# Kernel optimization log

Measured on AMD Instinct MI355X. Metric: run time of the kernel, lower is better.

## Reference

```python
import jax, jax.numpy as jnp
import numpy as np
import math

H = 16
LORA_SCALING = 16 / 8  # alpha / r
NEG_INF = -1e30

def _alibi_slopes(n_heads):
    start = 2.0 ** (-(2.0 ** (-(math.log2(n_heads) - 3))))
    return jnp.asarray([start * start ** i for i in range(n_heads)], dtype=jnp.float32)

def setup_inputs() -> dict:
    key = jax.random.key(0)
    ks = jax.random.split(key, 11)
    B, T, E, r = 4, 2048, 1024, 8
    d = {
        'x':  jax.random.normal(ks[0], (B, T, E), jnp.float32),
        'Wq': jax.random.normal(ks[1], (E, E), jnp.float32) * (E ** -0.5),
        'Aq': jax.random.normal(ks[2], (E, r), jnp.float32) * 0.01,
        'Bq': jax.random.normal(ks[3], (r, E), jnp.float32) * 0.01,
        'Wk': jax.random.normal(ks[4], (E, E), jnp.float32) * (E ** -0.5),
        'Ak': jax.random.normal(ks[5], (E, r), jnp.float32) * 0.01,
        'Bk': jax.random.normal(ks[6], (r, E), jnp.float32) * 0.01,
        'Wv': jax.random.normal(ks[7], (E, E), jnp.float32) * (E ** -0.5),
        'Av': jax.random.normal(ks[8], (E, r), jnp.float32) * 0.01,
        'Bv': jax.random.normal(ks[9], (r, E), jnp.float32) * 0.01,
        'Wp': jax.random.normal(ks[10], (E, E), jnp.float32) * (E ** -0.5),
    }
    return d

def _lora(x, W, A, Bm):
    # nn.Linear: x @ W.T ; LoRA: x @ B.T @ A.T * scaling
    return x @ W.T + ((x @ Bm.T) @ A.T) * LORA_SCALING

def reference(x, Wq, Aq, Bq, Wk, Ak, Bk, Wv, Av, Bv, Wp):
    B, T, E = x.shape
    dh = E // H
    q = _lora(x, Wq, Aq, Bq).reshape(B, T, H, dh).transpose(0, 2, 1, 3)  # [B,H,T,dh]
    k = _lora(x, Wk, Ak, Bk).reshape(B, T, H, dh).transpose(0, 2, 1, 3)
    v = _lora(x, Wv, Av, Bv).reshape(B, T, H, dh).transpose(0, 2, 1, 3)
    s = jnp.einsum('bhqd,bhkd->bhqk', q, k) / jnp.sqrt(jnp.float32(dh))
    i = jnp.arange(T)[:, None]
    j = jnp.arange(T)[None, :]
    slopes = _alibi_slopes(H)
    bias = slopes[:, None, None] * (i - j).astype(jnp.float32)  # [H,T,T]
    s = s + bias[None]
    s = jnp.where(j[None, None] <= i[None, None], s, NEG_INF)  # causal mask
    out = jnp.einsum('bhqk,bhkd->bhqd', jax.nn.softmax(s, axis=-1), v)
    out = out.transpose(0, 2, 1, 3).reshape(B, T, E)
    return out @ Wp.T  # dropout is identity in eval
```

## Files before the change

kernel.cpp:

```cpp
#include <hip/hip_runtime.h>

typedef unsigned short u16;
typedef unsigned int u32;
typedef u16  u16x8 __attribute__((ext_vector_type(8)));
typedef u16  u16x4 __attribute__((ext_vector_type(4)));
typedef u32  u32x4 __attribute__((ext_vector_type(4)));
typedef __bf16 bf16x2 __attribute__((ext_vector_type(2)));
typedef __bf16 bf16x8 __attribute__((ext_vector_type(8)));
typedef float f32x4 __attribute__((ext_vector_type(4)));
typedef float f32x16 __attribute__((ext_vector_type(16)));

__constant__ int KBW[16]  = {0,1,1,2,3,5,7,10,14,20,28,40,56,80,113,160};

__constant__ unsigned char RANKTBL[256] = {
  0xBF,0xCF,0xDF,0xEF,0xFF,
  0xBE,0xCE,0xDE,0xEE,0xFE,
  0xAE,0xAF,
  0xAD,0xBD,0xCD,0xDD,0xED,0xFD,
  0xAC,0xBC,0xCC,0xDC,0xEC,0xFC,
  0xAB,0xBB,0xCB,0xDB,0xEB,0xFB,
  0xAA,0xBA,0xCA,0xDA,0xEA,0xFA,
  0x9A,0x9B,0x9C,0x9D,0x9E,0x9F,
  0x99,0xA9,0xB9,0xC9,0xD9,0xE9,0xF9,
  0x98,0xA8,0xB8,0xC8,0xD8,0xE8,0xF8,
  0x97,0xA7,0xB7,0xC7,0xD7,0xE7,0xF7,
  0x87,0x88,0x89,0x8A,0x8B,0x8C,0x8D,0x8E,0x8F,
  0x86,0x96,0xA6,0xB6,0xC6,0xD6,0xE6,0xF6,
  0x85,0x95,0xA5,0xB5,0xC5,0xD5,0xE5,0xF5,
  0x75,0x76,0x77,0x78,0x79,0x7A,0x7B,0x7C,0x7D,0x7E,0x7F,
  0x74,0x84,0x94,0xA4,0xB4,0xC4,0xD4,0xE4,0xF4,
  0x63,0x64,0x65,0x66,0x67,0x68,0x69,0x6A,0x6B,0x6C,0x6D,0x6E,0x6F,
  0x73,0x83,0x93,0xA3,0xB3,0xC3,0xD3,0xE3,0xF3,
  0x52,0x53,0x54,0x55,0x56,0x57,0x58,0x59,0x5A,0x5B,0x5C,0x5D,0x5E,0x5F,
  0x62,0x72,0x82,0x92,0xA2,0xB2,0xC2,0xD2,0xE2,0xF2,
  0x41,0x42,0x43,0x44,0x45,0x46,0x47,0x48,0x49,0x4A,0x4B,0x4C,0x4D,0x4E,0x4F,
  0x51,0x61,0x71,0x81,0x91,0xA1,0xB1,0xC1,0xD1,0xE1,0xF1,
  0x31,0x32,0x33,0x34,0x35,0x36,0x37,0x38,0x39,0x3A,0x3B,0x3C,0x3D,0x3E,0x3F,
  0x10,0x11,0x12,0x13,0x14,0x15,0x16,0x17,0x18,0x19,0x1A,0x1B,0x1C,0x1D,0x1E,0x1F,
  0x20,0x21,0x22,0x23,0x24,0x25,0x26,0x27,0x28,0x29,0x2A,0x2B,0x2C,0x2D,0x2E,0x2F,
  0x30,0x40,0x50,0x60,0x70,0x80,0x90,0xA0,0xB0,0xC0,0xD0,0xE0,0xF0,
  0x00,0x01,0x02,0x03,0x04,0x05,0x06,0x07,0x08,0x09,0x0A,0x0B,0x0C,0x0D,0x0E,0x0F
};

static __device__ __forceinline__ u16 f2bf(float f) {
  unsigned int u = __float_as_uint(f);
  u += 0x7FFFu + ((u >> 16) & 1u);
  return (u16)(u >> 16);
}

static __device__ __forceinline__ u32 packbf(float a, float b) {
  bf16x2 t;
  t[0] = (__bf16)a;
  t[1] = (__bf16)b;
  return __builtin_bit_cast(u32, t);
}

static __device__ __forceinline__ f32x4 mfma16(bf16x8 a, bf16x8 b, f32x4 c) {
  return __builtin_amdgcn_mfma_f32_16x16x32_bf16(a, b, c, 0, 0, 0);
}
static __device__ __forceinline__ f32x16 mfma32(bf16x8 a, bf16x8 b, f32x16 c) {
  return __builtin_amdgcn_mfma_f32_32x32x16_bf16(a, b, c, 0, 0, 0);
}

static __device__ __forceinline__ void gload16(const void* g, void* lds) {
  __builtin_amdgcn_global_load_lds(
      (const __attribute__((address_space(1))) unsigned int*)g,
      (__attribute__((address_space(3))) unsigned int*)lds, 16, 0, 0);
}

__global__ __launch_bounds__(256) void k_cast_x(const float* __restrict__ in,
                                                u16* __restrict__ out) {
  size_t i = (size_t)blockIdx.x * 256 + threadIdx.x;
  const float4* p = reinterpret_cast<const float4*>(in) + i * 2;
  float4 a = p[0], b = p[1];
  u16x8 r;
  r[0] = f2bf(a.x); r[1] = f2bf(a.y); r[2] = f2bf(a.z); r[3] = f2bf(a.w);
  r[4] = f2bf(b.x); r[5] = f2bf(b.y); r[6] = f2bf(b.z); r[7] = f2bf(b.w);
  *reinterpret_cast<u16x8*>(out + i * 8) = r;
}

__global__ __launch_bounds__(256) void k_fold_w(
    const float* __restrict__ Wq, const float* __restrict__ Aq, const float* __restrict__ Bq,
    const float* __restrict__ Wk, const float* __restrict__ Ak, const float* __restrict__ Bk,
    const float* __restrict__ Wv, const float* __restrict__ Av, const float* __restrict__ Bv,
    const float* __restrict__ Wp, u16* __restrict__ wqkv, u16* __restrict__ wp) {
  int n = blockIdx.x;
  int widx = n >> 10, nr = n & 1023;
  const float *W, *A, *Bm; u16* dst;
  if (widx == 0)      { W = Wq; A = Aq; Bm = Bq; dst = wqkv; }
  else if (widx == 1) { W = Wk; A = Ak; Bm = Bk; dst = wqkv + (1 << 20); }
  else if (widx == 2) { W = Wv; A = Av; Bm = Bv; dst = wqkv + (2 << 20); }
  else                { W = Wp; A = nullptr; Bm = nullptr; dst = wp; }
  int e0 = threadIdx.x * 4;
  float4 w = *reinterpret_cast<const float4*>(W + (size_t)nr * 1024 + e0);
  if (widx < 3) {
    float acx = 0.f, acy = 0.f, acz = 0.f, acw = 0.f;
#pragma unroll
    for (int r = 0; r < 8; r++) {
      float ar = A[nr * 8 + r];
      float4 bm = *reinterpret_cast<const float4*>(Bm + (size_t)r * 1024 + e0);
      acx += ar * bm.x; acy += ar * bm.y; acz += ar * bm.z; acw += ar * bm.w;
    }
    w.x += 2.0f * acx; w.y += 2.0f * acy; w.z += 2.0f * acz; w.w += 2.0f * acw;
  }
  u16x4 r4; r4[0] = f2bf(w.x); r4[1] = f2bf(w.y); r4[2] = f2bf(w.z); r4[3] = f2bf(w.w);
  *reinterpret_cast<u16x4*>(dst + (size_t)nr * 1024 + e0) = r4;
}

template<int OUTF32>
__global__ __launch_bounds__(512) void k_gemm8(const u16* __restrict__ Ag,
                                               const u16* __restrict__ Bg,
                                               void* __restrict__ C,
                                               int K, int N, int lda, int gx) {
  __shared__ __align__(16) u16 As[2][8192];
  __shared__ __align__(16) u16 Bs[2][16384];
  const int tid = threadIdx.x;
  const int wid = tid >> 6, lane = tid & 63;
  const int l15 = lane & 15, lg = lane >> 4;
  const int wr = wid >> 2, wc = wid & 3;
  const int nwg = gridDim.x, cpx = nwg >> 3;
  const int bid = (int)blockIdx.x;
  const int sid = (bid & 7) * cpx + (bid >> 3);
  const int m0 = (sid % gx) * 128, n0 = (sid / gx) * 256;

  const int lrow = lane >> 3;
  const int lslot = lane & 7;

  f32x4 acc[4][4];
#pragma unroll
  for (int i = 0; i < 4; i++)
#pragma unroll
    for (int j = 0; j < 4; j++) acc[i][j] = (f32x4)0.0f;

  auto stageA = [&](int d, int t) {
#pragma unroll
    for (int i = 0; i < 2; i++) {
      int row = i * 64 + wid * 8 + lrow;
      int sc = (lslot ^ (row & 7)) << 3;
      gload16(Ag + (size_t)(m0 + row) * lda + t * 64 + sc,
              &As[d][(i * 64 + wid * 8) * 64]);
    }
  };
  auto stageB = [&](int d, int t) {
#pragma unroll
    for (int i = 0; i < 4; i++) {
      int row = i * 64 + wid * 8 + lrow;
      int sc = (lslot ^ (row & 7)) << 3;
      gload16(Bg + (size_t)(n0 + row) * K + t * 64 + sc,
              &Bs[d][(i * 64 + wid * 8) * 64]);
    }
  };
  auto ldsA = [&](int d, int m, int kk) {
    int rr = wr * 64 + m * 16 + l15;
    return *reinterpret_cast<const bf16x8*>(&As[d][rr * 64 + (((kk * 4 + lg) ^ (rr & 7)) << 3)]);
  };
  auto ldsB = [&](int d, int n, int kk) {
    int rr = wc * 64 + n * 16 + l15;
    return *reinterpret_cast<const bf16x8*>(&Bs[d][rr * 64 + (((kk * 4 + lg) ^ (rr & 7)) << 3)]);
  };

  bf16x8 fa[4][2], fb[4][2];
  auto quad = [&](int mh, int nh) {
    __builtin_amdgcn_s_setprio(1);
#pragma unroll
    for (int m = 0; m < 2; m++)
#pragma unroll
      for (int n = 0; n < 2; n++)
#pragma unroll
        for (int kk = 0; kk < 2; kk++)
          acc[mh * 2 + m][nh * 2 + n] =
              mfma16(fa[mh * 2 + m][kk], fb[nh * 2 + n][kk], acc[mh * 2 + m][nh * 2 + n]);
    __builtin_amdgcn_s_setprio(0);
  };

#define MIDBAR do { asm volatile("s_barrier" ::: "memory"); \
                    asm volatile("s_waitcnt lgkmcnt(0)" ::: "memory"); } while (0)
#define ENDBAR asm volatile("s_barrier" ::: "memory")

  stageB(0, 0); stageA(0, 0); stageB(1, 1); stageA(1, 1);
  asm volatile("s_waitcnt vmcnt(0)" ::: "memory");
  asm volatile("s_barrier" ::: "memory");

  const int niter = K >> 7;
  for (int it = 0; it < niter; ++it) {
    const bool st = (it + 1 < niter);
    const int T2 = 2 * it + 2;
#pragma unroll
    for (int d = 0; d < 2; ++d) {
#pragma unroll
      for (int m = 0; m < 2; m++)
#pragma unroll
        for (int kk = 0; kk < 2; kk++) fa[m][kk] = ldsA(d, m, kk);
#pragma unroll
      for (int n = 0; n < 2; n++)
#pragma unroll
        for (int kk = 0; kk < 2; kk++) fb[n][kk] = ldsB(d, n, kk);
      MIDBAR; quad(0, 0); ENDBAR;
#pragma unroll
      for (int n = 2; n < 4; n++)
#pragma unroll
        for (int kk = 0; kk < 2; kk++) fb[n][kk] = ldsB(d, n, kk);
      MIDBAR; quad(0, 1); ENDBAR;
#pragma unroll
      for (int m = 2; m < 4; m++)
#pragma unroll
        for (int kk = 0; kk < 2; kk++) fa[m][kk] = ldsA(d, m, kk);
      if (st) stageB(d, T2 + d);
      MIDBAR; quad(1, 1); ENDBAR;
      if (st) stageA(d, T2 + d);
      MIDBAR; quad(1, 0);
      if (st) asm volatile("s_waitcnt vmcnt(6)" ::: "memory");
      else    asm volatile("s_waitcnt vmcnt(0)" ::: "memory");
      ENDBAR;
    }
  }
#undef MIDBAR
#undef ENDBAR

  const int rbase = m0 + wr * 64, cbase = n0 + wc * 64;
#pragma unroll
  for (int m = 0; m < 4; m++)
#pragma unroll
    for (int n = 0; n < 4; n++)
#pragma unroll
      for (int j = 0; j < 4; j++) {
        int r  = rbase + m * 16 + lg * 4 + j;
        int cc = cbase + n * 16 + l15;
        if constexpr (OUTF32) {
          reinterpret_cast<float*>(C)[(size_t)r * N + cc] = acc[m][n][j];
        } else {
          reinterpret_cast<u16*>(C)[(size_t)r * N + cc] = f2bf(acc[m][n][j]);
        }
      }
}

__global__ __launch_bounds__(256) void k_vt(const u16* __restrict__ qkv,
                                            u16* __restrict__ vt) {
  __shared__ __align__(16) u16 tile[64 * 64];
  const int tb = blockIdx.x, h = blockIdx.y, b = blockIdx.z;
  const int tid = threadIdx.x;
  const size_t rb = (size_t)b * 2048;
  const int hv = 2048 + h * 64;
#pragma unroll
  for (int p = 0; p < 2; p++) {
    int r = p * 32 + (tid >> 3);
    int c = (tid & 7) * 8;
    u16x8 v = *reinterpret_cast<const u16x8*>(qkv + (rb + tb * 64 + r) * 3072 + hv + c);
    int slot = (c >> 3) ^ (r & 7) ^ ((r >> 3) & 7);
    *reinterpret_cast<u16x8*>(tile + r * 64 + slot * 8) = v;
  }
  __syncthreads();
#pragma unroll
  for (int p = 0; p < 2; p++) {
    int d = p * 32 + (tid >> 3);
    int t0 = (tid & 7) * 8;
    u16x8 v;
#pragma unroll
    for (int j = 0; j < 8; j++) {
      int r = t0 + j;
      int slot = (d >> 3) ^ (r & 7) ^ ((r >> 3) & 7);
      v[j] = tile[r * 64 + slot * 8 + (d & 7)];
    }
    *reinterpret_cast<u16x8*>(vt + ((size_t)(b * 16 + h) * 64 + d) * 2048 + tb * 64 + t0) = v;
  }
}

__global__ __launch_bounds__(256) void k_attn(const u16* __restrict__ qkv,
                                              const u16* __restrict__ vt,
                                              u16* __restrict__ aout) {
  __shared__ __align__(16) u16 Kl[2][64 * 64];
  __shared__ __align__(16) u16 Vl[2][64 * 64];
  const int tid = threadIdx.x, wave = tid >> 6, lane = tid & 63;
  const int l31 = lane & 31, half = lane >> 5;
  const int i = (int)blockIdx.x;
  const int b = i & 3, p = i >> 2;
  const int k4 = p >> 6, j4 = p & 63;
  const int ridx = (k4 == 0) ? j4 : (k4 == 1) ? 127 - j4 : (k4 == 2) ? 128 + j4 : 255 - j4;
  const int hqv = RANKTBL[ridx];
  const int h = hqv >> 4, qb = hqv & 15;
  const int rb = b * 2048;
  const int hq = h * 64, hk = 1024 + h * 64;
  const int bh64 = (b * 16 + h) * 64;
  const int qB = qb * 128;
  const int q0w = qB + wave * 32;
  const int q = q0w + l31;

  bf16x8 qf[4];
#pragma unroll
  for (int c = 0; c < 4; c++)
    qf[c] = *reinterpret_cast<const bf16x8*>(qkv + (size_t)(rb + q) * 3072 + hq + c * 16 + half * 8);

  const float slope2 = exp2f(-0.5f * (float)(h + 1)) * 1.44269504f;
  const float c0 = 0.18033688f;

  const int kend = min(2 * qb + 1, KBW[h]);

  float mrun = -1e30f, lrun = 0.f;
  f32x16 o0 = (f32x16)0.0f, o1 = (f32x16)0.0f;

  auto stage = [&](int kvr, int dst) {
#pragma unroll
    for (int i2 = 0; i2 < 2; i2++) {
      int row = (i2 * 4 + wave) * 8 + (lane >> 3);
      int scol = ((lane & 7) ^ (row & 7)) << 3;
      gload16(qkv + (size_t)(rb + kvr + row) * 3072 + hk + scol, &Kl[dst][(i2 * 4 + wave) * 512]);
      gload16(vt + (size_t)(bh64 + row) * 2048 + kvr + scol,     &Vl[dst][(i2 * 4 + wave) * 512]);
    }
  };

  stage(0, 0);
  __syncthreads();

  int bfi = 0;
  for (int kb = 0; kb <= kend; ++kb, bfi ^= 1) {
    const int kvr = kb * 64;
    if (kb < kend) stage(kvr + 64, bfi ^ 1);

    if (kvr <= q0w + 31) {
      f32x16 s[2];
#pragma unroll
      for (int t = 0; t < 2; t++) s[t] = (f32x16)0.0f;
      __builtin_amdgcn_s_setprio(1);
#pragma unroll
      for (int t = 0; t < 2; t++) {
        int r = t * 32 + l31;
#pragma unroll
        for (int cc = 0; cc < 4; cc++) {
          bf16x8 kf = *reinterpret_cast<const bf16x8*>(
              &Kl[bfi][r * 64 + (((cc * 2 + half) ^ (r & 7)) << 3)]);
          s[t] = mfma32(kf, qf[cc], s[t]);
        }
      }
      __builtin_amdgcn_s_setprio(0);

      const bool domask = (kvr + 63 > q0w);
      const int qrel = q - kvr - half * 4;
      const float qb0 = slope2 * (float)qrel;
      const float qb1 = qb0 - slope2 * 32.0f;
      float mt = -1e30f;
      if (domask) {
#pragma unroll
        for (int t = 0; t < 2; t++) {
          const float qbt = t ? qb1 : qb0;
          const int qmt = t ? (qrel - 32) : qrel;
#pragma unroll
          for (int r = 0; r < 16; r++) {
            const int krel = (r & 3) + 8 * (r >> 2);
            float val = fmaf(s[t][r], c0, fmaf(-slope2, (float)krel, qbt));
            val = (krel <= qmt) ? val : -3.0e38f;
            s[t][r] = val;
            mt = fmaxf(mt, val);
          }
        }
      } else {
#pragma unroll
        for (int t = 0; t < 2; t++) {
          const float qbt = t ? qb1 : qb0;
#pragma unroll
          for (int r = 0; r < 16; r += 2) {
            const int k0 = (r & 3) + 8 * (r >> 2);
            const int k1 = ((r + 1) & 3) + 8 * ((r + 1) >> 2);
            float v0 = fmaf(s[t][r],     c0, fmaf(-slope2, (float)k0, qbt));
            float v1 = fmaf(s[t][r + 1], c0, fmaf(-slope2, (float)k1, qbt));
            s[t][r] = v0; s[t][r + 1] = v1;
            mt = fmaxf(mt, fmaxf(v0, v1));
          }
        }
      }
      mt = fmaxf(mt, __shfl_xor(mt, 32));

      if (__any(mt - mrun > 8.0f)) {
        float mn = fmaxf(mrun, mt);
        float al = exp2f(mrun - mn);
        mrun = mn; lrun *= al;
#pragma unroll
        for (int r = 0; r < 16; r++) { o0[r] *= al; o1[r] *= al; }
      }

      float rs0 = 0.f, rs1 = 0.f;
#pragma unroll
      for (int t = 0; t < 2; t++)
#pragma unroll
        for (int r = 0; r < 16; r++) {
          float pp = exp2f(s[t][r] - mrun);
          s[t][r] = pp;
          if (t) rs1 += pp; else rs0 += pp;
        }
      float rs = rs0 + rs1;
      rs += __shfl_xor(rs, 32);
      lrun += rs;

      bf16x8 pf[4];
#pragma unroll
      for (int t = 0; t < 2; t++)
#pragma unroll
        for (int hs = 0; hs < 2; hs++) {
          u32 A0 = packbf(s[t][8 * hs + 0], s[t][8 * hs + 1]);
          u32 B0 = packbf(s[t][8 * hs + 2], s[t][8 * hs + 3]);
          u32 C0 = packbf(s[t][8 * hs + 4], s[t][8 * hs + 5]);
          u32 D0 = packbf(s[t][8 * hs + 6], s[t][8 * hs + 7]);
          asm volatile("v_permlane32_swap_b32 %0, %1" : "+v"(A0), "+v"(C0));
          asm volatile("v_permlane32_swap_b32 %0, %1" : "+v"(B0), "+v"(D0));
          u32x4 fr; fr[0] = A0; fr[1] = B0; fr[2] = C0; fr[3] = D0;
          pf[t * 2 + hs] = __builtin_bit_cast(bf16x8, fr);
        }

      __builtin_amdgcn_s_setprio(1);
#pragma unroll
      for (int dblk = 0; dblk < 2; dblk++) {
        int r = dblk * 32 + l31;
#pragma unroll
        for (int kc = 0; kc < 4; kc++) {
          bf16x8 vf = *reinterpret_cast<const bf16x8*>(
              &Vl[bfi][r * 64 + (((kc * 2 + half) ^ (r & 7)) << 3)]);
          if (dblk) o1 = mfma32(vf, pf[kc], o1);
          else      o0 = mfma32(vf, pf[kc], o0);
        }
      }
      __builtin_amdgcn_s_setprio(0);
    }
    __syncthreads();
  }

  const float linv = 1.0f / lrun;
#pragma unroll
  for (int dblk = 0; dblk < 2; dblk++)
#pragma unroll
    for (int rg = 0; rg < 4; rg++) {
      int d0 = dblk * 32 + 8 * rg + 4 * half;
      u16x4 r4;
#pragma unroll
      for (int j = 0; j < 4; j++) {
        float v = (dblk ? o1[rg * 4 + j] : o0[rg * 4 + j]) * linv;
        r4[j] = f2bf(v);
      }
      *reinterpret_cast<u16x4*>(aout + (size_t)(rb + q) * 3072 + hq + d0) = r4;
    }
}

extern "C" void kernel_launch(void* const* d_in, const int* in_sizes, int n_in,
                              void* d_out, int out_size, void* d_ws, size_t ws_size,
                              hipStream_t stream) {
  (void)in_sizes; (void)n_in; (void)out_size; (void)ws_size;
  const float* x  = (const float*)d_in[0];
  const float* Wq = (const float*)d_in[1];
  const float* Aq = (const float*)d_in[2];
  const float* Bq = (const float*)d_in[3];
  const float* Wk = (const float*)d_in[4];
  const float* Ak = (const float*)d_in[5];
  const float* Bk = (const float*)d_in[6];
  const float* Wv = (const float*)d_in[7];
  const float* Av = (const float*)d_in[8];
  const float* Bv = (const float*)d_in[9];
  const float* Wp = (const float*)d_in[10];

  char* ws = (char*)d_ws;
  u16* xb   = (u16*)(ws);
  u16* wqkv = (u16*)(ws + 16777216);
  u16* wp   = (u16*)(ws + 23068672);
  u16* qkv  = (u16*)(ws + 25165824);
  u16* vt   = xb;
  float* out = (float*)d_out;

  k_cast_x<<<dim3(4096), dim3(256), 0, stream>>>(x, xb);
  k_fold_w<<<dim3(4096), dim3(256), 0, stream>>>(Wq, Aq, Bq, Wk, Ak, Bk, Wv, Av, Bv, Wp, wqkv, wp);
  k_gemm8<0><<<dim3(768), dim3(512), 0, stream>>>(xb, wqkv, (void*)qkv, 1024, 3072, 1024, 64);
  k_vt<<<dim3(32, 16, 4), dim3(256), 0, stream>>>(qkv, vt);
  k_attn<<<dim3(1024), dim3(256), 0, stream>>>(qkv, vt, qkv);
  k_gemm8<1><<<dim3(256), dim3(512), 0, stream>>>(qkv, wp, (void*)out, 1024, 1024, 3072, 64);
}
```

Measured before the change: 184.1 us.

## Restructure GEMM main loop into two-phase per-tile schedule with staggered A/B prefetch

Replaces the four-quadrant-per-buffer main loop with a per-K-tile loop of two halves. All A fragments are loaded once per tile and reused across both halves of the B columns. B is prefetched one tile ahead and A two tiles ahead, so there are fewer barriers per tile and the vmcnt waits are tighter. This cuts LDS reads of A and barrier overhead, but the staggered prefetch distances make the buffer-reuse ordering more delicate.

New measurement: 182.6 us. No clear change (-0.8%).

```diff
diff --git a/kernel.cpp b/kernel.cpp
--- a/kernel.cpp
+++ b/kernel.cpp
@@ -159,60 +159,56 @@
     return *reinterpret_cast<const bf16x8*>(&Bs[d][rr * 64 + (((kk * 4 + lg) ^ (rr & 7)) << 3)]);
   };
 
-  bf16x8 fa[4][2], fb[4][2];
-  auto quad = [&](int mh, int nh) {
-    __builtin_amdgcn_s_setprio(1);
-#pragma unroll
-    for (int m = 0; m < 2; m++)
-#pragma unroll
-      for (int n = 0; n < 2; n++)
-#pragma unroll
-        for (int kk = 0; kk < 2; kk++)
-          acc[mh * 2 + m][nh * 2 + n] =
-              mfma16(fa[mh * 2 + m][kk], fb[nh * 2 + n][kk], acc[mh * 2 + m][nh * 2 + n]);
-    __builtin_amdgcn_s_setprio(0);
-  };
-
 #define MIDBAR do { asm volatile("s_barrier" ::: "memory"); \
                     asm volatile("s_waitcnt lgkmcnt(0)" ::: "memory"); } while (0)
 #define ENDBAR asm volatile("s_barrier" ::: "memory")
 
-  stageB(0, 0); stageA(0, 0); stageB(1, 1); stageA(1, 1);
-  asm volatile("s_waitcnt vmcnt(0)" ::: "memory");
+  stageB(0, 0); stageA(0, 0); stageA(1, 1);
+  asm volatile("s_waitcnt vmcnt(2)" ::: "memory");
   asm volatile("s_barrier" ::: "memory");
 
-  const int niter = K >> 7;
-  for (int it = 0; it < niter; ++it) {
-    const bool st = (it + 1 < niter);
-    const int T2 = 2 * it + 2;
-#pragma unroll
-    for (int d = 0; d < 2; ++d) {
-#pragma unroll
-      for (int m = 0; m < 2; m++)
-#pragma unroll
-        for (int kk = 0; kk < 2; kk++) fa[m][kk] = ldsA(d, m, kk);
+  bf16x8 fa[4][2], fb[2][2];
+  const int nt = K >> 6;
+  for (int t = 0; t < nt; ++t) {
+    const int d = t & 1;
+#pragma unroll
+    for (int m = 0; m < 4; m++)
+#pragma unroll
+      for (int kk = 0; kk < 2; kk++) fa[m][kk] = ldsA(d, m, kk);
+#pragma unroll
+    for (int n = 0; n < 2; n++)
+#pragma unroll
+      for (int kk = 0; kk < 2; kk++) fb[n][kk] = ldsB(d, n, kk);
+    if (t + 1 < nt) stageB(d ^ 1, t + 1);
+    MIDBAR;
+    __builtin_amdgcn_s_setprio(1);
+#pragma unroll
+    for (int m = 0; m < 4; m++)
 #pragma unroll
       for (int n = 0; n < 2; n++)
 #pragma unroll
-        for (int kk = 0; kk < 2; kk++) fb[n][kk] = ldsB(d, n, kk);
-      MIDBAR; quad(0, 0); ENDBAR;
-#pragma unroll
-      for (int n = 2; n < 4; n++)
-#pragma unroll
-        for (int kk = 0; kk < 2; kk++) fb[n][kk] = ldsB(d, n, kk);
-      MIDBAR; quad(0, 1); ENDBAR;
-#pragma unroll
-      for (int m = 2; m < 4; m++)
-#pragma unroll
-        for (int kk = 0; kk < 2; kk++) fa[m][kk] = ldsA(d, m, kk);
-      if (st) stageB(d, T2 + d);
-      MIDBAR; quad(1, 1); ENDBAR;
-      if (st) stageA(d, T2 + d);
-      MIDBAR; quad(1, 0);
-      if (st) asm volatile("s_waitcnt vmcnt(6)" ::: "memory");
-      else    asm volatile("s_waitcnt vmcnt(0)" ::: "memory");
-      ENDBAR;
-    }
+        for (int kk = 0; kk < 2; kk++)
+          acc[m][n] = mfma16(fa[m][kk], fb[n][kk], acc[m][n]);
+    __builtin_amdgcn_s_setprio(0);
+    ENDBAR;
+#pragma unroll
+    for (int n = 0; n < 2; n++)
+#pragma unroll
+      for (int kk = 0; kk < 2; kk++) fb[n][kk] = ldsB(d, n + 2, kk);
+    if (t + 2 < nt) stageA(d, t + 2);
+    MIDBAR;
+    __builtin_amdgcn_s_setprio(1);
+#pragma unroll
+    for (int m = 0; m < 4; m++)
+#pragma unroll
+      for (int n = 0; n < 2; n++)
+#pragma unroll
+        for (int kk = 0; kk < 2; kk++)
+          acc[m][n + 2] = mfma16(fa[m][kk], fb[n][kk], acc[m][n + 2]);
+    __builtin_amdgcn_s_setprio(0);
+    if (t + 2 < nt) asm volatile("s_waitcnt vmcnt(2)" ::: "memory");
+    else            asm volatile("s_waitcnt vmcnt(0)" ::: "memory");
+    ENDBAR;
   }
 #undef MIDBAR
 #undef ENDBAR
```
